# Kernel optimization log

Hardware: AMD Instinct MI355X
Metric: run time of the kernel (lower is better)

The kernel has to match this reference:

```python
import jax, jax.numpy as jnp
import numpy as np

B, L, E, H = 128, 256, 512, 512
N_TRANS = 2  # n_layers - 1 TGRU transition layers per direction


def _gru_cell(gx, h, Uh, m):
    """Generic GRU-style cell update.
    gx: input-side pre-activations (incl. bias), [B,3H] or [3H] (TGRU: bias only).
    h:  previous hidden [B,H]; Uh: [H,3H]; m: mask [B].
    Gate order along last dim: (r, z, h_tilde).
    """
    gh = h @ Uh  # [B,3H]
    g = gx + gh
    r = jax.nn.sigmoid(g[:, :H])
    z = jax.nn.sigmoid(g[:, H:2 * H])
    # reset gate applies to the hidden contribution only
    ht = jnp.tanh((gx + jnp.zeros_like(gh))[:, 2 * H:] + r * gh[:, 2 * H:])
    hn = (1.0 - z) * ht + z * h
    mm = m[:, None]
    return mm * hn + (1.0 - mm) * h


def _direction_scan(xs_t, m_t, Wx, Uh, b, tU, tb, reverse):
    """Run LGRU + stacked TGRUs over time. xs_t: [L,B,E], m_t: [L,B]."""
    h0 = jnp.zeros((xs_t.shape[1], H), dtype=xs_t.dtype)

    def step(h, xm):
        x, m = xm
        h = _gru_cell(x @ Wx + b, h, Uh, m)          # LGRU (input-fed)
        for i in range(N_TRANS):                      # TGRUs (transition, no input)
            h = _gru_cell(tb[i], h, tU[i], m)
        return h, h

    _, anns = jax.lax.scan(step, h0, (xs_t, m_t), reverse=reverse)
    return anns  # [L,B,H], time-aligned with input order


def setup_inputs() -> dict:
    key = jax.random.key(0)
    ks = jax.random.split(key, 12)
    s_in = 1.0 / np.sqrt(E)
    s_h = 1.0 / np.sqrt(H)
    inp = {
        "xs": jax.random.normal(ks[0], (B, L, E), dtype=jnp.float32),
        "xs_mask": jnp.ones((B, L), dtype=jnp.float32),
        # forward-direction LGRU
        "f_Wx": jax.random.normal(ks[1], (E, 3 * H), dtype=jnp.float32) * s_in,
        "f_Uh": jax.random.normal(ks[2], (H, 3 * H), dtype=jnp.float32) * s_h,
        "f_b": jnp.zeros((3 * H,), dtype=jnp.float32),
        # backward-direction LGRU
        "b_Wx": jax.random.normal(ks[3], (E, 3 * H), dtype=jnp.float32) * s_in,
        "b_Uh": jax.random.normal(ks[4], (H, 3 * H), dtype=jnp.float32) * s_h,
        "b_b": jnp.zeros((3 * H,), dtype=jnp.float32),
        # stacked TGRU transition layers (N_TRANS per direction)
        "f_tU": jax.random.normal(ks[5], (N_TRANS, H, 3 * H), dtype=jnp.float32) * s_h,
        "f_tb": jnp.zeros((N_TRANS, 3 * H), dtype=jnp.float32),
        "b_tU": jax.random.normal(ks[6], (N_TRANS, H, 3 * H), dtype=jnp.float32) * s_h,
        "b_tb": jnp.zeros((N_TRANS, 3 * H), dtype=jnp.float32),
    }
    return inp


def reference(xs, xs_mask, f_Wx, f_Uh, f_b, b_Wx, b_Uh, b_b, f_tU, f_tb, b_tU, b_tb):
    xs_t = jnp.swapaxes(xs, 0, 1)       # [L,B,E]
    m_t = jnp.swapaxes(xs_mask, 0, 1)   # [L,B]
    r_anns = _direction_scan(xs_t, m_t, f_Wx, f_Uh, f_b, f_tU, f_tb, reverse=False)
    l_anns = _direction_scan(xs_t, m_t, b_Wx, b_Uh, b_b, b_tU, b_tb, reverse=True)
    ann = jnp.concatenate([r_anns, l_anns], axis=-1)  # [L,B,2H]
    ann = jnp.swapaxes(ann, 0, 1)                     # [B,L,2H]
    return ann * xs_mask[:, :, None]
```

## Files before the change

kernel.cpp:

```cpp
#include <hip/hip_runtime.h>
#include <cstdint>

typedef __attribute__((ext_vector_type(8))) short short8;
typedef __attribute__((ext_vector_type(4))) float f32x4;
typedef __attribute__((ext_vector_type(4))) unsigned int u32x4;

#define L_ 256
#define E_ 512
#define H_ 512
#define TH_ 1536

#define PACK_PER_CS 24576
#define PACK_TOTAL (8 * 32 * PACK_PER_CS)
#define HPUB_OFF ((size_t)PACK_TOTAL * 2)
#define GRP_DW 16384
#define BUF_DW (8 * GRP_DW)

#define BAIL_TICKS 50000000ULL
#define FAST_POLL 24
#define FAST_BULK 3

__device__ __forceinline__ unsigned short f2bf(float v) {
    unsigned int u = __builtin_bit_cast(unsigned int, v);
    u += 0x7FFFu + ((u >> 16) & 1u);
    return (unsigned short)(u >> 16);
}
__device__ __forceinline__ float sigm_(float x) { return 1.f / (1.f + __expf(-x)); }
__device__ __forceinline__ float tanh_(float x) {
    float e = __expf(2.f * x);
    return 1.f - 2.f / (e + 1.f);
}

__global__ void pack_weights(const float* __restrict__ fWx, const float* __restrict__ fUh,
                             const float* __restrict__ ftU, const float* __restrict__ bWx,
                             const float* __restrict__ bUh, const float* __restrict__ btU,
                             unsigned short* __restrict__ pack) {
    unsigned int idx = blockIdx.x * 256u + threadIdx.x;
    if (idx >= (unsigned)PACK_TOTAL) return;
    int e = idx & 7;
    int l = (idx >> 3) & 63;
    unsigned int r = idx >> 9;
    int f = r % 3; r /= 3;
    int ks = r & 15; r >>= 4;
    int cs = r & 31; r >>= 5;
    int m = r;
    int k = ks * 32 + (l >> 4) * 8 + e;
    int col = f * 512 + cs * 16 + (l & 15);
    const float* src;
    switch (m) {
        case 0: src = fWx; break;
        case 1: src = fUh; break;
        case 2: src = ftU; break;
        case 3: src = ftU + H_ * TH_; break;
        case 4: src = bWx; break;
        case 5: src = bUh; break;
        case 6: src = btU; break;
        default: src = btU + H_ * TH_; break;
    }
    pack[idx] = f2bf(src[(size_t)k * TH_ + col]);
}

__device__ __forceinline__ void poll_tag(const unsigned int* sp, unsigned int tag, bool* dead) {
    if (*dead) return;
    for (int it = 0; it < FAST_POLL; ++it) {
        unsigned int v;
        asm volatile("global_load_dword %0, %1, off sc1" : "=v"(v) : "v"(sp) : "memory");
        asm volatile("s_waitcnt vmcnt(0)" ::: "memory");
        __builtin_amdgcn_sched_barrier(0);
        if (__all((int)((v >> 16) >= tag))) return;
    }
    unsigned long long t0 = __builtin_amdgcn_s_memrealtime();
    while (true) {
        unsigned int v;
        asm volatile("global_load_dword %0, %1, off sc0 sc1" : "=v"(v) : "v"(sp) : "memory");
        asm volatile("s_waitcnt vmcnt(0)" ::: "memory");
        __builtin_amdgcn_sched_barrier(0);
        if (__all((int)((v >> 16) >= tag))) return;
        if (__builtin_amdgcn_s_memrealtime() - t0 > BAIL_TICKS) { *dead = true; return; }
    }
}

template <bool SYS>
__device__ __forceinline__ void ld32(const unsigned int* base, u32x4* D) {
#pragma unroll
    for (int i = 0; i < 32; ++i) {
        if constexpr (SYS)
            asm volatile("global_load_dwordx4 %0, %1, off offset:%c2 sc0 sc1"
                         : "=v"(D[i]) : "v"(base), "i"(((i >> 1) * 128) + ((i & 1) * 16)) : "memory");
        else
            asm volatile("global_load_dwordx4 %0, %1, off offset:%c2 sc1"
                         : "=v"(D[i]) : "v"(base), "i"(((i >> 1) * 128) + ((i & 1) * 16)) : "memory");
    }
    asm volatile("s_waitcnt vmcnt(0)" ::: "memory");
    __builtin_amdgcn_sched_barrier(0);
}

__device__ __forceinline__ bool chk(const u32x4* D, unsigned int ehi) {
    unsigned int acc = 0;
#pragma unroll
    for (int i = 0; i < 32; ++i) {
#pragma unroll
        for (int e = 0; e < 4; ++e) acc |= D[i][e] ^ ehi;
    }
    return __all((int)((acc & 0xFFFF0000u) == 0u));
}

__device__ __forceinline__ void load_htag(const unsigned int* base, unsigned int tag, u32x4* D,
                                          bool* dead) {
    const unsigned int ehi = tag << 16;
    if (!*dead) {
        for (int it = 0; it < FAST_BULK; ++it) {
            ld32<false>(base, D);
            if (chk(D, ehi)) return;
        }
        unsigned long long t0 = __builtin_amdgcn_s_memrealtime();
        while (true) {
            ld32<true>(base, D);
            if (chk(D, ehi)) return;
            if (__builtin_amdgcn_s_memrealtime() - t0 > BAIL_TICKS) { *dead = true; break; }
        }
    }
    const unsigned int p = ehi | 0x7FC0u;
#pragma unroll
    for (int i = 0; i < 32; ++i) { D[i][0] = p; D[i][1] = p; D[i][2] = p; D[i][3] = p; }
}

__device__ __forceinline__ short8 pack_a(const u32x4& d0, const u32x4& d1) {
    u32x4 r;
    r[0] = __builtin_amdgcn_perm(d0[1], d0[0], 0x05040100u);
    r[1] = __builtin_amdgcn_perm(d0[3], d0[2], 0x05040100u);
    r[2] = __builtin_amdgcn_perm(d1[1], d1[0], 0x05040100u);
    r[3] = __builtin_amdgcn_perm(d1[3], d1[2], 0x05040100u);
    return __builtin_bit_cast(short8, r);
}

__device__ __forceinline__ void st_tag(unsigned int* p, unsigned int v) {
    asm volatile("global_store_dword %0, %1, off sc0 sc1" :: "v"(p), "v"(v) : "memory");
}

__device__ __forceinline__ void trans_cell(const unsigned int* hbase, const unsigned int* spp,
                                           unsigned int tag, const unsigned short* ldsp,
                                           int lane, float br, float bz, float bhh,
                                           const float* mm, float* hreg, unsigned int* hwr,
                                           int rc0g, int hcol, bool* dead) {
    poll_tag(spp, tag, dead);
    u32x4 D[32];
    load_htag(hbase, tag, D, dead);
    f32x4 acc0 = {0.f, 0.f, 0.f, 0.f}, acc1 = acc0, acc2 = acc0;
#pragma unroll
    for (int ks = 0; ks < 16; ++ks) {
        short8 A = pack_a(D[2 * ks], D[2 * ks + 1]);
        short8 B0 = *(const short8*)(ldsp + (ks * 3 + 0) * 512 + lane * 8);
        short8 B1 = *(const short8*)(ldsp + (ks * 3 + 1) * 512 + lane * 8);
        short8 B2 = *(const short8*)(ldsp + (ks * 3 + 2) * 512 + lane * 8);
        acc0 = __builtin_amdgcn_mfma_f32_16x16x32_bf16(A, B0, acc0, 0, 0, 0);
        acc1 = __builtin_amdgcn_mfma_f32_16x16x32_bf16(A, B1, acc1, 0, 0, 0);
        acc2 = __builtin_amdgcn_mfma_f32_16x16x32_bf16(A, B2, acc2, 0, 0, 0);
    }
    const unsigned int ptag = (tag + 1) << 16;
#pragma unroll
    for (int j = 0; j < 4; ++j) {
        float r = sigm_(acc0[j] + br);
        float z = sigm_(acc1[j] + bz);
        float ht = tanh_(bhh + r * acc2[j]);
        float hn = (1.f - z) * ht + z * hreg[j];
        hn = mm[j] * hn + (1.f - mm[j]) * hreg[j];
        hreg[j] = hn;
        st_tag(hwr + (rc0g + j) * 512 + hcol, ptag | (unsigned int)f2bf(hn));
    }
}

__global__ __launch_bounds__(128, 1) void rnn_kernel(
    const float* __restrict__ xs, const float* __restrict__ xmask,
    const float* __restrict__ fb, const float* __restrict__ bb,
    const float* __restrict__ ftb, const float* __restrict__ btb,
    float* __restrict__ out, const unsigned short* __restrict__ pack,
    unsigned int* __restrict__ hpub32) {
    extern __shared__ unsigned short lds_u16[];
    const int tid = threadIdx.x;
    const int wg = blockIdx.x;
    const int g = wg & 7;
    const int cs = wg >> 3;
    const int dir = g >> 2;
    const int qb = g & 3;
    const int w = tid >> 6;
    const int lane = tid & 63;

    for (int m = 0; m < 3; ++m) {
        const u32x4* src = (const u32x4*)(pack + (size_t)((dir * 4 + 1 + m) * 32 + cs) * PACK_PER_CS);
        u32x4* dst = (u32x4*)(lds_u16 + m * PACK_PER_CS);
        for (int i = tid; i < PACK_PER_CS / 8; i += 128) dst[i] = src[i];
    }
    __syncthreads();

    const int c16 = lane & 15;
    const int kg = lane >> 4;
    const int rowAg = w * 16 + c16;
    const int rc0g = w * 16 + kg * 4;
    const int rowA = qb * 32 + rowAg;
    const int rowC0 = qb * 32 + rc0g;
    const int hcol = cs * 16 + c16;

    const float* bsrc = dir ? bb : fb;
    const float* tbsrc = dir ? btb : ftb;
    const float b0r = bsrc[hcol], b0z = bsrc[512 + hcol], b0h = bsrc[1024 + hcol];
    const float b1r = tbsrc[hcol], b1z = tbsrc[512 + hcol], b1h = tbsrc[1024 + hcol];
    const float b2r = tbsrc[TH_ + hcol], b2z = tbsrc[TH_ + 512 + hcol], b2h = tbsrc[TH_ + 1024 + hcol];

    float hreg[4] = {0.f, 0.f, 0.f, 0.f};
    bool dead = false;

    const unsigned short* wxpack =
        pack + (size_t)((dir * 4 + 0) * 32 + cs) * PACK_PER_CS + lane * 8;
    unsigned int* hb0 = hpub32 + 0 * BUF_DW + g * GRP_DW;
    unsigned int* hb1 = hpub32 + 1 * BUF_DW + g * GRP_DW;
    const int ka = kg * 8;
    const int aoff = rowAg * 512 + ka;
    const float* xrow = xs + (size_t)rowA * L_ * E_ + ka;

    const int sp_hi = lane >> 5;
    const int sp_off = (w * 16 + (sp_hi ? 15 : 3)) * 512 + (lane & 31) * 16 + (sp_hi ? 15 : 0);

    unsigned int gcnt = 0;
    for (int s = 0; s < L_; ++s) {
        const int t = dir ? (L_ - 1 - s) : s;
        float mm[4];
#pragma unroll
        for (int j = 0; j < 4; ++j) mm[j] = xmask[(rowC0 + j) * L_ + t];

        f32x4 acc0 = {0.f, 0.f, 0.f, 0.f}, acc1 = acc0, accgx = acc0;
        {
            const float* xp = xrow + (size_t)t * E_;
#pragma unroll
            for (int ks = 0; ks < 16; ++ks) {
                f32x4 x0 = *(const f32x4*)(xp + ks * 32);
                f32x4 x1 = *(const f32x4*)(xp + ks * 32 + 4);
                short8 A2;
#pragma unroll
                for (int e = 0; e < 4; ++e) {
                    A2[e] = (short)f2bf(x0[e]);
                    A2[4 + e] = (short)f2bf(x1[e]);
                }
                short8 W0 = *(const short8*)(wxpack + (ks * 3 + 0) * 512);
                short8 W1 = *(const short8*)(wxpack + (ks * 3 + 1) * 512);
                short8 W2 = *(const short8*)(wxpack + (ks * 3 + 2) * 512);
                acc0 = __builtin_amdgcn_mfma_f32_16x16x32_bf16(A2, W0, acc0, 0, 0, 0);
                acc1 = __builtin_amdgcn_mfma_f32_16x16x32_bf16(A2, W1, acc1, 0, 0, 0);
                accgx = __builtin_amdgcn_mfma_f32_16x16x32_bf16(A2, W2, accgx, 0, 0, 0);
            }
        }
        {
            const unsigned int* hbcur = (gcnt & 1) ? hb1 : hb0;
            unsigned int* hwr = (gcnt & 1) ? hb0 : hb1;
            poll_tag(hbcur + sp_off, gcnt, &dead);
            u32x4 D[32];
            load_htag(hbcur + aoff, gcnt, D, &dead);
            f32x4 accgh = {0.f, 0.f, 0.f, 0.f};
#pragma unroll
            for (int ks = 0; ks < 16; ++ks) {
                short8 A = pack_a(D[2 * ks], D[2 * ks + 1]);
                short8 B0 = *(const short8*)(lds_u16 + (ks * 3 + 0) * 512 + lane * 8);
                short8 B1 = *(const short8*)(lds_u16 + (ks * 3 + 1) * 512 + lane * 8);
                short8 B2 = *(const short8*)(lds_u16 + (ks * 3 + 2) * 512 + lane * 8);
                acc0 = __builtin_amdgcn_mfma_f32_16x16x32_bf16(A, B0, acc0, 0, 0, 0);
                acc1 = __builtin_amdgcn_mfma_f32_16x16x32_bf16(A, B1, acc1, 0, 0, 0);
                accgh = __builtin_amdgcn_mfma_f32_16x16x32_bf16(A, B2, accgh, 0, 0, 0);
            }
            const unsigned int ptag = (gcnt + 1) << 16;
#pragma unroll
            for (int j = 0; j < 4; ++j) {
                float r = sigm_(acc0[j] + b0r);
                float z = sigm_(acc1[j] + b0z);
                float ht = tanh_(accgx[j] + b0h + r * accgh[j]);
                float hn = (1.f - z) * ht + z * hreg[j];
                hn = mm[j] * hn + (1.f - mm[j]) * hreg[j];
                hreg[j] = hn;
                st_tag(hwr + (rc0g + j) * 512 + hcol, ptag | (unsigned int)f2bf(hn));
            }
        }
        gcnt++;
        trans_cell(((gcnt & 1) ? hb1 : hb0) + aoff, ((gcnt & 1) ? hb1 : hb0) + sp_off, gcnt,
                   lds_u16 + PACK_PER_CS, lane, b1r, b1z, b1h, mm, hreg,
                   (gcnt & 1) ? hb0 : hb1, rc0g, hcol, &dead);
        gcnt++;
        trans_cell(((gcnt & 1) ? hb1 : hb0) + aoff, ((gcnt & 1) ? hb1 : hb0) + sp_off, gcnt,
                   lds_u16 + 2 * PACK_PER_CS, lane, b2r, b2z, b2h, mm, hreg,
                   (gcnt & 1) ? hb0 : hb1, rc0g, hcol, &dead);
        gcnt++;
#pragma unroll
        for (int j = 0; j < 4; ++j) {
            out[(size_t)((rowC0 + j) * L_ + t) * 1024 + dir * 512 + hcol] = mm[j] * hreg[j];
        }
    }
}

extern "C" void kernel_launch(void* const* d_in, const int* in_sizes, int n_in, void* d_out,
                              int out_size, void* d_ws, size_t ws_size, hipStream_t stream) {
    (void)in_sizes; (void)n_in; (void)out_size; (void)ws_size;
    const float* xs = (const float*)d_in[0];
    const float* xmask = (const float*)d_in[1];
    const float* fWx = (const float*)d_in[2];
    const float* fUh = (const float*)d_in[3];
    const float* fb = (const float*)d_in[4];
    const float* bWx = (const float*)d_in[5];
    const float* bUh = (const float*)d_in[6];
    const float* bb = (const float*)d_in[7];
    const float* ftU = (const float*)d_in[8];
    const float* ftb = (const float*)d_in[9];
    const float* btU = (const float*)d_in[10];
    const float* btb = (const float*)d_in[11];

    unsigned short* pack = (unsigned short*)d_ws;
    unsigned int* hpub32 = (unsigned int*)((char*)d_ws + HPUB_OFF);

    hipMemsetAsync((char*)d_ws + HPUB_OFF, 0, (size_t)2 * BUF_DW * 4, stream);

    pack_weights<<<PACK_TOTAL / 256, 256, 0, stream>>>(fWx, fUh, ftU, bWx, bUh, btU, pack);

    hipFuncSetAttribute((const void*)rnn_kernel, hipFuncAttributeMaxDynamicSharedMemorySize,
                        3 * PACK_PER_CS * 2);

    rnn_kernel<<<256, 128, 3 * PACK_PER_CS * 2, stream>>>(xs, xmask, fb, bb, ftb, btb,
                                                          (float*)d_out, pack, hpub32);
}
```

Before: 4.802 ms.

## Drop sentinel polling and speculatively prefetch tagged hidden state before input GEMM

Removes the separate sentinel-tag poll and the fast non-coherent retry loads, and instead issues the system-coherent bulk load of the tagged hidden state right away, checking tags after it lands. In the LGRU step the hidden-state load is issued before the input-projection MFMA loop, so its latency overlaps that compute. If the data is not ready when it arrives, the whole 32-load bulk is reissued in the spin loop. Each retry now costs a full bulk load instead of a single dword, which adds memory traffic under contention.

```diff
diff --git a/kernel.cpp b/kernel.cpp
--- a/kernel.cpp
+++ b/kernel.cpp
@@ -17,8 +17,6 @@
 #define BUF_DW (8 * GRP_DW)
 
 #define BAIL_TICKS 50000000ULL
-#define FAST_POLL 24
-#define FAST_BULK 3
 
 __device__ __forceinline__ unsigned short f2bf(float v) {
     unsigned int u = __builtin_bit_cast(unsigned int, v);
@@ -60,62 +58,35 @@
     pack[idx] = f2bf(src[(size_t)k * TH_ + col]);
 }
 
-__device__ __forceinline__ void poll_tag(const unsigned int* sp, unsigned int tag, bool* dead) {
-    if (*dead) return;
-    for (int it = 0; it < FAST_POLL; ++it) {
-        unsigned int v;
-        asm volatile("global_load_dword %0, %1, off sc1" : "=v"(v) : "v"(sp) : "memory");
-        asm volatile("s_waitcnt vmcnt(0)" ::: "memory");
-        __builtin_amdgcn_sched_barrier(0);
-        if (__all((int)((v >> 16) >= tag))) return;
-    }
-    unsigned long long t0 = __builtin_amdgcn_s_memrealtime();
-    while (true) {
-        unsigned int v;
-        asm volatile("global_load_dword %0, %1, off sc0 sc1" : "=v"(v) : "v"(sp) : "memory");
-        asm volatile("s_waitcnt vmcnt(0)" ::: "memory");
-        __builtin_amdgcn_sched_barrier(0);
-        if (__all((int)((v >> 16) >= tag))) return;
-        if (__builtin_amdgcn_s_memrealtime() - t0 > BAIL_TICKS) { *dead = true; return; }
-    }
-}
-
-template <bool SYS>
-__device__ __forceinline__ void ld32(const unsigned int* base, u32x4* D) {
+__device__ __forceinline__ void ld32_issue(const unsigned int* base, u32x4* D) {
+#pragma unroll
+    for (int i = 0; i < 32; ++i)
+        asm volatile("global_load_dwordx4 %0, %1, off offset:%c2 sc0 sc1"
+                     : "=v"(D[i]) : "v"(base), "i"(((i >> 1) * 128) + ((i & 1) * 16)) : "memory");
+}
+
+__device__ __forceinline__ bool chk(const u32x4* D, unsigned int ehi) {
+    unsigned int acc = 0;
 #pragma unroll
     for (int i = 0; i < 32; ++i) {
-        if constexpr (SYS)
-            asm volatile("global_load_dwordx4 %0, %1, off offset:%c2 sc0 sc1"
-                         : "=v"(D[i]) : "v"(base), "i"(((i >> 1) * 128) + ((i & 1) * 16)) : "memory");
-        else
-            asm volatile("global_load_dwordx4 %0, %1, off offset:%c2 sc1"
-                         : "=v"(D[i]) : "v"(base), "i"(((i >> 1) * 128) + ((i & 1) * 16)) : "memory");
-    }
+#pragma unroll
+        for (int e = 0; e < 4; ++e) acc |= D[i][e] ^ ehi;
+    }
+    return __all((int)((acc & 0xFFFF0000u) == 0u));
+}
+
+__device__ __forceinline__ void wait_verify(const unsigned int* base, unsigned int tag,
+                                            u32x4* D, bool* dead) {
+    const unsigned int ehi = tag << 16;
     asm volatile("s_waitcnt vmcnt(0)" ::: "memory");
     __builtin_amdgcn_sched_barrier(0);
-}
-
-__device__ __forceinline__ bool chk(const u32x4* D, unsigned int ehi) {
-    unsigned int acc = 0;
-#pragma unroll
-    for (int i = 0; i < 32; ++i) {
-#pragma unroll
-        for (int e = 0; e < 4; ++e) acc |= D[i][e] ^ ehi;
-    }
-    return __all((int)((acc & 0xFFFF0000u) == 0u));
-}
-
-__device__ __forceinline__ void load_htag(const unsigned int* base, unsigned int tag, u32x4* D,
-                                          bool* dead) {
-    const unsigned int ehi = tag << 16;
+    if (chk(D, ehi)) return;
     if (!*dead) {
-        for (int it = 0; it < FAST_BULK; ++it) {
-            ld32<false>(base, D);
-            if (chk(D, ehi)) return;
-        }
         unsigned long long t0 = __builtin_amdgcn_s_memrealtime();
         while (true) {
-            ld32<true>(base, D);
+            ld32_issue(base, D);
+            asm volatile("s_waitcnt vmcnt(0)" ::: "memory");
+            __builtin_amdgcn_sched_barrier(0);
             if (chk(D, ehi)) return;
             if (__builtin_amdgcn_s_memrealtime() - t0 > BAIL_TICKS) { *dead = true; break; }
         }
@@ -138,14 +109,13 @@
     asm volatile("global_store_dword %0, %1, off sc0 sc1" :: "v"(p), "v"(v) : "memory");
 }
 
-__device__ __forceinline__ void trans_cell(const unsigned int* hbase, const unsigned int* spp,
-                                           unsigned int tag, const unsigned short* ldsp,
-                                           int lane, float br, float bz, float bhh,
-                                           const float* mm, float* hreg, unsigned int* hwr,
-                                           int rc0g, int hcol, bool* dead) {
-    poll_tag(spp, tag, dead);
+__device__ __forceinline__ void trans_cell(const unsigned int* hbase, unsigned int tag,
+                                           const unsigned short* ldsp, int lane, float br,
+                                           float bz, float bhh, const float* mm, float* hreg,
+                                           unsigned int* hwr, int rc0g, int hcol, bool* dead) {
     u32x4 D[32];
-    load_htag(hbase, tag, D, dead);
+    ld32_issue(hbase, D);
+    wait_verify(hbase, tag, D, dead);
     f32x4 acc0 = {0.f, 0.f, 0.f, 0.f}, acc1 = acc0, acc2 = acc0;
 #pragma unroll
     for (int ks = 0; ks < 16; ++ks) {
@@ -218,9 +188,6 @@
     const int aoff = rowAg * 512 + ka;
     const float* xrow = xs + (size_t)rowA * L_ * E_ + ka;
 
-    const int sp_hi = lane >> 5;
-    const int sp_off = (w * 16 + (sp_hi ? 15 : 3)) * 512 + (lane & 31) * 16 + (sp_hi ? 15 : 0);
-
     unsigned int gcnt = 0;
     for (int s = 0; s < L_; ++s) {
         const int t = dir ? (L_ - 1 - s) : s;
@@ -228,33 +195,33 @@
 #pragma unroll
         for (int j = 0; j < 4; ++j) mm[j] = xmask[(rowC0 + j) * L_ + t];
 
-        f32x4 acc0 = {0.f, 0.f, 0.f, 0.f}, acc1 = acc0, accgx = acc0;
         {
-            const float* xp = xrow + (size_t)t * E_;
-#pragma unroll
-            for (int ks = 0; ks < 16; ++ks) {
-                f32x4 x0 = *(const f32x4*)(xp + ks * 32);
-                f32x4 x1 = *(const f32x4*)(xp + ks * 32 + 4);
-                short8 A2;
-#pragma unroll
-                for (int e = 0; e < 4; ++e) {
-                    A2[e] = (short)f2bf(x0[e]);
-                    A2[4 + e] = (short)f2bf(x1[e]);
+            const unsigned int* hbcur = ((gcnt & 1) ? hb1 : hb0) + aoff;
+            unsigned int* hwr = (gcnt & 1) ? hb0 : hb1;
+            u32x4 D[32];
+            ld32_issue(hbcur, D);
+            f32x4 acc0 = {0.f, 0.f, 0.f, 0.f}, acc1 = acc0, accgx = acc0;
+            {
+                const float* xp = xrow + (size_t)t * E_;
+#pragma unroll
+                for (int ks = 0; ks < 16; ++ks) {
+                    f32x4 x0 = *(const f32x4*)(xp + ks * 32);
+                    f32x4 x1 = *(const f32x4*)(xp + ks * 32 + 4);
+                    short8 A2;
+#pragma unroll
+                    for (int e = 0; e < 4; ++e) {
+                        A2[e] = (short)f2bf(x0[e]);
+                        A2[4 + e] = (short)f2bf(x1[e]);
+                    }
+                    short8 W0 = *(const short8*)(wxpack + (ks * 3 + 0) * 512);
+                    short8 W1 = *(const short8*)(wxpack + (ks * 3 + 1) * 512);
+                    short8 W2 = *(const short8*)(wxpack + (ks * 3 + 2) * 512);
+                    acc0 = __builtin_amdgcn_mfma_f32_16x16x32_bf16(A2, W0, acc0, 0, 0, 0);
+                    acc1 = __builtin_amdgcn_mfma_f32_16x16x32_bf16(A2, W1, acc1, 0, 0, 0);
+                    accgx = __builtin_amdgcn_mfma_f32_16x16x32_bf16(A2, W2, accgx, 0, 0, 0);
                 }
-                short8 W0 = *(const short8*)(wxpack + (ks * 3 + 0) * 512);
-                short8 W1 = *(const short8*)(wxpack + (ks * 3 + 1) * 512);
-                short8 W2 = *(const short8*)(wxpack + (ks * 3 + 2) * 512);
-                acc0 = __builtin_amdgcn_mfma_f32_16x16x32_bf16(A2, W0, acc0, 0, 0, 0);
-                acc1 = __builtin_amdgcn_mfma_f32_16x16x32_bf16(A2, W1, acc1, 0, 0, 0);
-                accgx = __builtin_amdgcn_mfma_f32_16x16x32_bf16(A2, W2, accgx, 0, 0, 0);
             }
-        }
-        {
-            const unsigned int* hbcur = (gcnt & 1) ? hb1 : hb0;
-            unsigned int* hwr = (gcnt & 1) ? hb0 : hb1;
-            poll_tag(hbcur + sp_off, gcnt, &dead);
-            u32x4 D[32];
-            load_htag(hbcur + aoff, gcnt, D, &dead);
+            wait_verify(hbcur, gcnt, D, &dead);
             f32x4 accgh = {0.f, 0.f, 0.f, 0.f};
 #pragma unroll
             for (int ks = 0; ks < 16; ++ks) {
@@ -279,13 +246,11 @@
             }
         }
         gcnt++;
-        trans_cell(((gcnt & 1) ? hb1 : hb0) + aoff, ((gcnt & 1) ? hb1 : hb0) + sp_off, gcnt,
-                   lds_u16 + PACK_PER_CS, lane, b1r, b1z, b1h, mm, hreg,
-                   (gcnt & 1) ? hb0 : hb1, rc0g, hcol, &dead);
+        trans_cell(((gcnt & 1) ? hb1 : hb0) + aoff, gcnt, lds_u16 + PACK_PER_CS, lane,
+                   b1r, b1z, b1h, mm, hreg, (gcnt & 1) ? hb0 : hb1, rc0g, hcol, &dead);
         gcnt++;
-        trans_cell(((gcnt & 1) ? hb1 : hb0) + aoff, ((gcnt & 1) ? hb1 : hb0) + sp_off, gcnt,
-                   lds_u16 + 2 * PACK_PER_CS, lane, b2r, b2z, b2h, mm, hreg,
-                   (gcnt & 1) ? hb0 : hb1, rc0g, hcol, &dead);
+        trans_cell(((gcnt & 1) ? hb1 : hb0) + aoff, gcnt, lds_u16 + 2 * PACK_PER_CS, lane,
+                   b2r, b2z, b2h, mm, hreg, (gcnt & 1) ? hb0 : hb1, rc0g, hcol, &dead);
         gcnt++;
 #pragma unroll
         for (int j = 0; j < 4; ++j) {
```

Result: slower. 7.183 ms (+49.6%).
